# Kernel tuning notes

Hardware: AMD Instinct MI355X
Metric: run time of the kernel (lower is better)

Reference implementation:

```python
import jax, jax.numpy as jnp
import numpy as np

EMBED_DIM = 1024
NUM_HEADS = 16
HEAD_DIM = EMBED_DIM // NUM_HEADS


def setup_inputs() -> dict:
    key = jax.random.key(0)
    k_x, k_qw, k_qb, k_ow, k_ob = jax.random.split(key, 5)
    B, T, C = 2, 2048, EMBED_DIM
    scale = 1.0 / np.sqrt(C)
    return {
        "x": jax.random.normal(k_x, (B, T, C), dtype=jnp.float32),
        "qkv_w": jax.random.normal(k_qw, (C, 3 * C), dtype=jnp.float32) * scale,
        "qkv_b": jax.random.normal(k_qb, (3 * C,), dtype=jnp.float32) * 0.02,
        "out_w": jax.random.normal(k_ow, (C, C), dtype=jnp.float32) * scale,
        "out_b": jax.random.normal(k_ob, (C,), dtype=jnp.float32) * 0.02,
    }


def reference(x, qkv_w, qkv_b, out_w, out_b):
    # x: (B, T, C). Causal masked multi-head self-attention (eval mode: dropout off).
    B, T, C = x.shape
    H, Dh = NUM_HEADS, HEAD_DIM
    qkv = x @ qkv_w + qkv_b                      # (B, T, 3C)
    qkv = qkv.reshape(B, T, 3, H, Dh)
    q = jnp.transpose(qkv[:, :, 0], (0, 2, 1, 3))  # (B, H, T, Dh)
    k = jnp.transpose(qkv[:, :, 1], (0, 2, 1, 3))
    v = jnp.transpose(qkv[:, :, 2], (0, 2, 1, 3))
    scores = jnp.einsum("bhqd,bhkd->bhqk", q, k) / np.sqrt(Dh)
    causal = jnp.tril(jnp.ones((T, T), dtype=bool))
    scores = jnp.where(causal[None, None], scores, -jnp.inf)
    attn = jax.nn.softmax(scores, axis=-1)        # (B, H, T, T)
    out = jnp.einsum("bhqk,bhkd->bhqd", attn, v)  # (B, H, T, Dh)
    out = jnp.transpose(out, (0, 2, 1, 3)).reshape(B, T, C)
    return out @ out_w + out_b
```

## Files before the change

kernel.cpp:

```cpp
#include <hip/hip_runtime.h>


typedef __bf16 bf16;
typedef __attribute__((ext_vector_type(4))) __bf16 bf16x4;
typedef __attribute__((ext_vector_type(8))) __bf16 bf16x8;
typedef __attribute__((ext_vector_type(4))) float f32x4;

#define T_SEQ 2048
#define NHEAD 16
#define QSCALE 0.1803368801111244f

__device__ __forceinline__ void async16(const bf16* g, const bf16* l) {
    __builtin_amdgcn_global_load_lds(
        (const __attribute__((address_space(1))) void*)g,
        (__attribute__((address_space(3))) void*)l, 16, 0, 0);
}

__global__ __launch_bounds__(256) void prep(
    const float* __restrict__ x, bf16* __restrict__ xb,
    const float* __restrict__ qkv_w, bf16* __restrict__ wbT,
    const float* __restrict__ out_w, bf16* __restrict__ owbT) {
    const int bid = blockIdx.x, tid = threadIdx.x;
    if (bid < 4096) {
        int i = (bid * 256 + tid) * 4;
        float4 v = *(const float4*)(x + i);
        bf16x4 o;
        o.x = (bf16)v.x; o.y = (bf16)v.y; o.z = (bf16)v.z; o.w = (bf16)v.w;
        *(bf16x4*)(xb + i) = o;
        return;
    }
    __shared__ float tile[32][33];
    const float* in;
    bf16* out;
    int K_, N_, b;
    if (bid < 7168) { b = bid - 4096; in = qkv_w; out = wbT; K_ = 1024; N_ = 3072; }
    else            { b = bid - 7168; in = out_w; out = owbT; K_ = 1024; N_ = 1024; }
    int k0 = (b & 31) * 32, n0 = (b >> 5) * 32;
    int tx = tid & 31, ty = tid >> 5;
    for (int r = 0; r < 32; r += 8)
        tile[ty + r][tx] = in[(k0 + ty + r) * N_ + n0 + tx];
    __syncthreads();
    for (int r = 0; r < 32; r += 8)
        out[(n0 + ty + r) * K_ + k0 + tx] = (bf16)tile[tx][ty + r];
}


__global__ __launch_bounds__(256) void gemm_qkv(
    const bf16* __restrict__ A, const bf16* __restrict__ Bt,
    const float* __restrict__ bias,
    bf16* __restrict__ Qo, bf16* __restrict__ Ko, bf16* __restrict__ Vt) {
    __shared__ __align__(16) bf16 As[128 * 32];
    __shared__ __align__(16) bf16 Bs[128 * 32];
    const int t = threadIdx.x;
    const int lane = t & 63, wave = t >> 6;
    const int l15 = lane & 15, quad = lane >> 4;
    const int wm = wave & 1, wn = wave >> 1;
    const int m0 = blockIdx.y * 128, n0 = blockIdx.x * 128;

    f32x4 acc[4][4] = {};

    const bf16* ag = A + (m0 + (t >> 2)) * 1024 + (t & 3) * 8;
    const bf16* bg = Bt + (n0 + (t >> 2)) * 1024 + (t & 3) * 8;
    bf16* as0 = As + wave * 512;
    bf16* as1 = As + 2048 + wave * 512;
    bf16* bs0 = Bs + wave * 512;
    bf16* bs1 = Bs + 2048 + wave * 512;

    for (int k0 = 0; k0 < 1024; k0 += 32) {
        async16(ag + k0, as0);
        async16(ag + 64 * 1024 + k0, as1);
        async16(bg + k0, bs0);
        async16(bg + 64 * 1024 + k0, bs1);
        __syncthreads();
        bf16x8 af[4], bfr[4];
        for (int i = 0; i < 4; i++)
            af[i] = *(const bf16x8*)(As + (wm * 64 + i * 16 + l15) * 32 + quad * 8);
        for (int j = 0; j < 4; j++)
            bfr[j] = *(const bf16x8*)(Bs + (wn * 64 + j * 16 + l15) * 32 + quad * 8);
        for (int i = 0; i < 4; i++)
            for (int j = 0; j < 4; j++)
                acc[i][j] = __builtin_amdgcn_mfma_f32_16x16x32_bf16(af[i], bfr[j], acc[i][j], 0, 0, 0);
        __syncthreads();
    }

    for (int i = 0; i < 4; i++) {
        for (int j = 0; j < 4; j++) {
            int col = n0 + wn * 64 + j * 16 + l15;
            float bv = bias[col];
            int sec = col >> 10, c2 = col & 1023, h = c2 >> 6, d = c2 & 63;
            for (int r = 0; r < 4; r++) {
                int row = m0 + wm * 64 + i * 16 + quad * 4 + r;
                int b = row >> 11, tt = row & 2047;
                int bh = b * NHEAD + h;
                float v = acc[i][j][r] + bv;
                if (sec == 0)
                    Qo[(bh * T_SEQ + tt) * 64 + d] = (bf16)(v * QSCALE);
                else if (sec == 1)
                    Ko[(bh * T_SEQ + tt) * 64 + d] = (bf16)v;
                else
                    Vt[(bh * 64 + d) * T_SEQ + tt] = (bf16)v;
            }
        }
    }
}

#define PSTR 64
__global__ __launch_bounds__(512, 2) void attn(
    const bf16* __restrict__ Q, const bf16* __restrict__ K,
    const bf16* __restrict__ Vt, bf16* __restrict__ AO) {
    __shared__ __align__(16) bf16 Ks[2][64 * 64];
    __shared__ __align__(16) bf16 Vs[2][64 * 64];
    __shared__ __align__(16) bf16 Pb[8][16 * PSTR];
    const int tid = threadIdx.x;
    const int lane = tid & 63, wave = tid >> 6;
    const int l15 = lane & 15, quad = lane >> 4;
    const int bh = ((blockIdx.x & 7) << 2) | ((blockIdx.x >> 3) & 3);
    const int pr = blockIdx.x >> 5;

    const bf16* kp = K + bh * T_SEQ * 64;
    const bf16* vp = Vt + bh * 64 * T_SEQ;
    bf16* pw = &Pb[wave][0];
    const int b_ = bh >> 4, h_ = bh & 15;

    const int sx = (quad ^ (l15 & 7)) << 3;

    auto stage = [&](int kb, int b) {
        int rowi = tid >> 3, p = tid & 7;
        const bf16* ksrc = kp + (kb + rowi) * 64 + ((p ^ (rowi & 7)) << 3);
        async16(ksrc, &Ks[b][wave * 512]);
        const bf16* vsrc = vp + rowi * T_SEQ + kb + ((p ^ (rowi & 7)) << 3);
        async16(vsrc, &Vs[b][wave * 512]);
    };

    for (int half = 0; half < 2; half++) {
        const int qt = half ? pr : (15 - pr);
        const int t0 = qt * 128 + wave * 16;
        const int m = t0 >> 4;
        const bf16* qp = Q + (bh * T_SEQ + t0) * 64;
        bf16x8 qf0 = *(const bf16x8*)(qp + l15 * 64 + quad * 8);
        bf16x8 qf1 = *(const bf16x8*)(qp + l15 * 64 + 32 + quad * 8);

        f32x4 acc[4] = {};
        float lsum[4] = {0.f, 0.f, 0.f, 0.f};

        const int C = 2 * qt + 2;
        stage(0, 0);
        for (int c = 0; c < C; c++) {
            __syncthreads();
            if (c + 1 < C) stage((c + 1) * 64, (c + 1) & 1);
            const int nr = m - 4 * c + 1;
            if (nr > 0) {
                const int na = min(4, nr);
                const bool dg = (nr <= 4);
                const bf16* ksb = &Ks[c & 1][0];
                const bf16* vsb = &Vs[c & 1][0];

                f32x4 sc[4];
                for (int n = 0; n < 4; n++) {
                    if (n < na) {
                        const bf16* kbase = ksb + (n * 16 + l15) * 64;
                        bf16x8 kf0 = *(const bf16x8*)(kbase + sx);
                        bf16x8 kf1 = *(const bf16x8*)(kbase + (sx ^ 32));
                        f32x4 z = {};
                        z = __builtin_amdgcn_mfma_f32_16x16x32_bf16(qf0, kf0, z, 0, 0, 0);
                        z = __builtin_amdgcn_mfma_f32_16x16x32_bf16(qf1, kf1, z, 0, 0, 0);
                        sc[n] = z;
                    }
                }
                for (int n = 0; n < 4; n++) {
                    for (int r = 0; r < 4; r++) {
                        float e = 0.0f;
                        if (n < na) {
                            float v = sc[n][r];
                            if (dg && n == na - 1) {
                                int key = c * 64 + n * 16 + l15;
                                int qrow = t0 + quad * 4 + r;
                                if (key > qrow) v = -100000.0f;
                            }
                            e = __builtin_amdgcn_exp2f(v);
                        }
                        lsum[r] += e;
                        pw[(quad * 4 + r) * PSTR + n * 16 + l15] = (bf16)e;
                    }
                }
                __builtin_amdgcn_s_waitcnt(0xC07F);
                bf16x8 pf0 = *(const bf16x8*)(pw + l15 * PSTR + quad * 8);
                bf16x8 pf1 = *(const bf16x8*)(pw + l15 * PSTR + 32 + quad * 8);
                for (int j = 0; j < 4; j++) {
                    const bf16* vbase = vsb + (j * 16 + l15) * 64;
                    bf16x8 vf0 = *(const bf16x8*)(vbase + sx);
                    bf16x8 vf1 = *(const bf16x8*)(vbase + (sx ^ 32));
                    acc[j] = __builtin_amdgcn_mfma_f32_16x16x32_bf16(pf0, vf0, acc[j], 0, 0, 0);
                    acc[j] = __builtin_amdgcn_mfma_f32_16x16x32_bf16(pf1, vf1, acc[j], 0, 0, 0);
                }
            }
        }

        float linv[4];
        for (int r = 0; r < 4; r++) {
            float v = lsum[r];
            v += __shfl_xor(v, 1, 16);
            v += __shfl_xor(v, 2, 16);
            v += __shfl_xor(v, 4, 16);
            v += __shfl_xor(v, 8, 16);
            linv[r] = 1.0f / v;
        }
        bf16* aop = AO + (b_ * T_SEQ + t0) * 1024 + h_ * 64;
        for (int r = 0; r < 4; r++)
            for (int j = 0; j < 4; j++)
                aop[(quad * 4 + r) * 1024 + j * 16 + l15] = (bf16)(acc[j][r] * linv[r]);
    }
}

__global__ __launch_bounds__(256) void gemm_out_k(
    const bf16* __restrict__ A, const bf16* __restrict__ Bt,
    const float* __restrict__ bias, float* __restrict__ out) {
    __shared__ __align__(16) bf16 As[128 * 32];
    __shared__ __align__(16) bf16 Bs[128 * 32];
    const int t = threadIdx.x;
    const int lane = t & 63, wave = t >> 6;
    const int l15 = lane & 15, quad = lane >> 4;
    const int wm = wave & 1, wn = wave >> 1;
    const int m0 = blockIdx.y * 128, n0 = blockIdx.x * 128;

    f32x4 acc[4][4] = {};

    const bf16* ag = A + (m0 + (t >> 2)) * 1024 + (t & 3) * 8;
    const bf16* bg = Bt + (n0 + (t >> 2)) * 1024 + (t & 3) * 8;
    bf16* as0 = As + wave * 512;
    bf16* as1 = As + 2048 + wave * 512;
    bf16* bs0 = Bs + wave * 512;
    bf16* bs1 = Bs + 2048 + wave * 512;

    for (int k0 = 0; k0 < 1024; k0 += 32) {
        async16(ag + k0, as0);
        async16(ag + 64 * 1024 + k0, as1);
        async16(bg + k0, bs0);
        async16(bg + 64 * 1024 + k0, bs1);
        __syncthreads();
        bf16x8 af[4], bfr[4];
        for (int i = 0; i < 4; i++)
            af[i] = *(const bf16x8*)(As + (wm * 64 + i * 16 + l15) * 32 + quad * 8);
        for (int j = 0; j < 4; j++)
            bfr[j] = *(const bf16x8*)(Bs + (wn * 64 + j * 16 + l15) * 32 + quad * 8);
        for (int i = 0; i < 4; i++)
            for (int j = 0; j < 4; j++)
                acc[i][j] = __builtin_amdgcn_mfma_f32_16x16x32_bf16(af[i], bfr[j], acc[i][j], 0, 0, 0);
        __syncthreads();
    }

    for (int i = 0; i < 4; i++) {
        for (int j = 0; j < 4; j++) {
            int col = n0 + wn * 64 + j * 16 + l15;
            float bv = bias[col];
            for (int r = 0; r < 4; r++) {
                int row = m0 + wm * 64 + i * 16 + quad * 4 + r;
                out[row * 1024 + col] = acc[i][j][r] + bv;
            }
        }
    }
}

extern "C" void kernel_launch(void* const* d_in, const int* in_sizes, int n_in,
                              void* d_out, int out_size, void* d_ws, size_t ws_size,
                              hipStream_t stream) {
    const float* x     = (const float*)d_in[0];
    const float* qkv_w = (const float*)d_in[1];
    const float* qkv_b = (const float*)d_in[2];
    const float* out_w = (const float*)d_in[3];
    const float* out_b = (const float*)d_in[4];
    float* out = (float*)d_out;

    char* ws = (char*)d_ws;
    bf16* xb   = (bf16*)(ws);
    bf16* wbT  = (bf16*)(ws + (8ull << 20));
    bf16* owbT = (bf16*)(ws + (14ull << 20));
    bf16* Qb   = (bf16*)(ws + (16ull << 20));
    bf16* Kb   = (bf16*)(ws + (24ull << 20));
    bf16* Vt   = (bf16*)(ws + (32ull << 20));
    bf16* AO   = (bf16*)(ws + (40ull << 20));

    prep<<<8192, 256, 0, stream>>>(x, xb, qkv_w, wbT, out_w, owbT);
    gemm_qkv<<<dim3(24, 32), 256, 0, stream>>>(xb, wbT, qkv_b, Qb, Kb, Vt);
    attn<<<256, 512, 0, stream>>>(Qb, Kb, Vt, AO);
    gemm_out_k<<<dim3(8, 32), 256, 0, stream>>>(AO, owbT, out_b, out);
}
```

Measured before the change: 202.4 us.

## Split attention into 64-row query tiles with transposed score MFMA

The attention kernel now launches 1024 blocks of 256 threads, each owning one 64-row query tile, instead of 256 blocks of 512 threads that each processed two paired 128-row tiles. The score MFMA operands are swapped so each lane holds a key column, which lets the lane write probabilities as a packed bf16x4 into a padded LDS row and reduce row sums with two cross-quad shuffles. Diagonal blocks compute only the needed key subtiles per wave. This aims to raise occupancy and balance the causal workload at finer grain, at the cost of more K/V tile reloads per query row and more blocks to schedule.

```diff
diff --git a/kernel.cpp b/kernel.cpp
--- a/kernel.cpp
+++ b/kernel.cpp
@@ -43,7 +43,6 @@
     for (int r = 0; r < 32; r += 8)
         out[(n0 + ty + r) * K_ + k0 + tx] = (bf16)tile[tx][ty + r];
 }
-
 
 __global__ __launch_bounds__(256) void gemm_qkv(
     const bf16* __restrict__ A, const bf16* __restrict__ Bt,
@@ -104,111 +103,105 @@
     }
 }
 
-#define PSTR 64
-__global__ __launch_bounds__(512, 2) void attn(
+#define PST 80
+__global__ __launch_bounds__(256, 4) void attn(
     const bf16* __restrict__ Q, const bf16* __restrict__ K,
     const bf16* __restrict__ Vt, bf16* __restrict__ AO) {
     __shared__ __align__(16) bf16 Ks[2][64 * 64];
     __shared__ __align__(16) bf16 Vs[2][64 * 64];
-    __shared__ __align__(16) bf16 Pb[8][16 * PSTR];
+    __shared__ __align__(16) bf16 Pa[4][16 * PST];
     const int tid = threadIdx.x;
     const int lane = tid & 63, wave = tid >> 6;
     const int l15 = lane & 15, quad = lane >> 4;
-    const int bh = ((blockIdx.x & 7) << 2) | ((blockIdx.x >> 3) & 3);
-    const int pr = blockIdx.x >> 5;
+    const int xcdr = blockIdx.x & 7;
+    const int i_ = blockIdx.x >> 3;
+    const int bh = (xcdr << 2) | (i_ & 3);
+    const int ti = i_ >> 2;
+    const int qt = (ti & 1) ? (ti >> 1) : (31 - (ti >> 1));
+    const int t0w = qt * 64 + wave * 16;
 
     const bf16* kp = K + bh * T_SEQ * 64;
     const bf16* vp = Vt + bh * 64 * T_SEQ;
-    bf16* pw = &Pb[wave][0];
+    bf16* pw = &Pa[wave][0];
     const int b_ = bh >> 4, h_ = bh & 15;
 
     const int sx = (quad ^ (l15 & 7)) << 3;
 
+    const bf16* qp = Q + (bh * T_SEQ + t0w) * 64;
+    bf16x8 qf0 = *(const bf16x8*)(qp + l15 * 64 + quad * 8);
+    bf16x8 qf1 = *(const bf16x8*)(qp + l15 * 64 + 32 + quad * 8);
+
     auto stage = [&](int kb, int b) {
-        int rowi = tid >> 3, p = tid & 7;
-        const bf16* ksrc = kp + (kb + rowi) * 64 + ((p ^ (rowi & 7)) << 3);
-        async16(ksrc, &Ks[b][wave * 512]);
-        const bf16* vsrc = vp + rowi * T_SEQ + kb + ((p ^ (rowi & 7)) << 3);
-        async16(vsrc, &Vs[b][wave * 512]);
+        for (int i = 0; i < 2; i++) {
+            int row = i * 32 + (tid >> 3), p = tid & 7;
+            const bf16* ksrc = kp + (kb + row) * 64 + ((p ^ (row & 7)) << 3);
+            async16(ksrc, &Ks[b][i * 2048 + wave * 512]);
+            const bf16* vsrc = vp + row * T_SEQ + kb + ((p ^ (row & 7)) << 3);
+            async16(vsrc, &Vs[b][i * 2048 + wave * 512]);
+        }
     };
 
-    for (int half = 0; half < 2; half++) {
-        const int qt = half ? pr : (15 - pr);
-        const int t0 = qt * 128 + wave * 16;
-        const int m = t0 >> 4;
-        const bf16* qp = Q + (bh * T_SEQ + t0) * 64;
-        bf16x8 qf0 = *(const bf16x8*)(qp + l15 * 64 + quad * 8);
-        bf16x8 qf1 = *(const bf16x8*)(qp + l15 * 64 + 32 + quad * 8);
-
-        f32x4 acc[4] = {};
-        float lsum[4] = {0.f, 0.f, 0.f, 0.f};
-
-        const int C = 2 * qt + 2;
-        stage(0, 0);
-        for (int c = 0; c < C; c++) {
-            __syncthreads();
-            if (c + 1 < C) stage((c + 1) * 64, (c + 1) & 1);
-            const int nr = m - 4 * c + 1;
-            if (nr > 0) {
-                const int na = min(4, nr);
-                const bool dg = (nr <= 4);
-                const bf16* ksb = &Ks[c & 1][0];
-                const bf16* vsb = &Vs[c & 1][0];
-
-                f32x4 sc[4];
-                for (int n = 0; n < 4; n++) {
-                    if (n < na) {
-                        const bf16* kbase = ksb + (n * 16 + l15) * 64;
-                        bf16x8 kf0 = *(const bf16x8*)(kbase + sx);
-                        bf16x8 kf1 = *(const bf16x8*)(kbase + (sx ^ 32));
-                        f32x4 z = {};
-                        z = __builtin_amdgcn_mfma_f32_16x16x32_bf16(qf0, kf0, z, 0, 0, 0);
-                        z = __builtin_amdgcn_mfma_f32_16x16x32_bf16(qf1, kf1, z, 0, 0, 0);
-                        sc[n] = z;
-                    }
+    f32x4 acc[4] = {};
+    float lsum = 0.0f;
+
+    const int C = qt + 1;
+    stage(0, 0);
+    for (int c = 0; c < C; c++) {
+        __syncthreads();
+        if (c + 1 < C) stage((c + 1) * 64, (c + 1) & 1);
+        const bf16* ksb = &Ks[c & 1][0];
+        const bf16* vsb = &Vs[c & 1][0];
+        const bool dg = (c == qt);
+        const int na = dg ? (wave + 1) : 4;
+
+        f32x4 sc[4];
+        for (int n = 0; n < 4; n++) {
+            if (n < na) {
+                const bf16* kbase = ksb + (n * 16 + l15) * 64;
+                bf16x8 kf0 = *(const bf16x8*)(kbase + sx);
+                bf16x8 kf1 = *(const bf16x8*)(kbase + (sx ^ 32));
+                f32x4 z = {};
+                z = __builtin_amdgcn_mfma_f32_16x16x32_bf16(kf0, qf0, z, 0, 0, 0);
+                z = __builtin_amdgcn_mfma_f32_16x16x32_bf16(kf1, qf1, z, 0, 0, 0);
+                sc[n] = z;
+            }
+        }
+        for (int n = 0; n < 4; n++) {
+            bf16x4 pv;
+            if (n < na) {
+                const bool dmask = dg && (n == na - 1);
+                for (int r = 0; r < 4; r++) {
+                    float v = sc[n][r];
+                    if (dmask && (quad * 4 + r > l15)) v = -100000.0f;
+                    float e = __builtin_amdgcn_exp2f(v);
+                    lsum += e;
+                    pv[r] = (bf16)e;
                 }
-                for (int n = 0; n < 4; n++) {
-                    for (int r = 0; r < 4; r++) {
-                        float e = 0.0f;
-                        if (n < na) {
-                            float v = sc[n][r];
-                            if (dg && n == na - 1) {
-                                int key = c * 64 + n * 16 + l15;
-                                int qrow = t0 + quad * 4 + r;
-                                if (key > qrow) v = -100000.0f;
-                            }
-                            e = __builtin_amdgcn_exp2f(v);
-                        }
-                        lsum[r] += e;
-                        pw[(quad * 4 + r) * PSTR + n * 16 + l15] = (bf16)e;
-                    }
-                }
-                __builtin_amdgcn_s_waitcnt(0xC07F);
-                bf16x8 pf0 = *(const bf16x8*)(pw + l15 * PSTR + quad * 8);
-                bf16x8 pf1 = *(const bf16x8*)(pw + l15 * PSTR + 32 + quad * 8);
-                for (int j = 0; j < 4; j++) {
-                    const bf16* vbase = vsb + (j * 16 + l15) * 64;
-                    bf16x8 vf0 = *(const bf16x8*)(vbase + sx);
-                    bf16x8 vf1 = *(const bf16x8*)(vbase + (sx ^ 32));
-                    acc[j] = __builtin_amdgcn_mfma_f32_16x16x32_bf16(pf0, vf0, acc[j], 0, 0, 0);
-                    acc[j] = __builtin_amdgcn_mfma_f32_16x16x32_bf16(pf1, vf1, acc[j], 0, 0, 0);
-                }
-            }
-        }
-
-        float linv[4];
-        for (int r = 0; r < 4; r++) {
-            float v = lsum[r];
-            v += __shfl_xor(v, 1, 16);
-            v += __shfl_xor(v, 2, 16);
-            v += __shfl_xor(v, 4, 16);
-            v += __shfl_xor(v, 8, 16);
-            linv[r] = 1.0f / v;
-        }
-        bf16* aop = AO + (b_ * T_SEQ + t0) * 1024 + h_ * 64;
-        for (int r = 0; r < 4; r++)
-            for (int j = 0; j < 4; j++)
-                aop[(quad * 4 + r) * 1024 + j * 16 + l15] = (bf16)(acc[j][r] * linv[r]);
+            } else {
+                pv[0] = pv[1] = pv[2] = pv[3] = (bf16)0.0f;
+            }
+            *(bf16x4*)(pw + l15 * PST + n * 16 + quad * 4) = pv;
+        }
+        __builtin_amdgcn_s_waitcnt(0xC07F);
+        for (int g = 0; g < 2; g++) {
+            bf16x8 pf = *(const bf16x8*)(pw + l15 * PST + g * 32 + quad * 8);
+            for (int j = 0; j < 4; j++) {
+                const bf16* vbase = vsb + (j * 16 + l15) * 64;
+                bf16x8 vf = *(const bf16x8*)(vbase + (g ? (sx ^ 32) : sx));
+                acc[j] = __builtin_amdgcn_mfma_f32_16x16x32_bf16(pf, vf, acc[j], 0, 0, 0);
+            }
+        }
+    }
+
+    lsum += __shfl_xor(lsum, 16);
+    lsum += __shfl_xor(lsum, 32);
+    float linv = 1.0f / lsum;
+
+    bf16* aop = AO + (b_ * T_SEQ + t0w) * 1024 + h_ * 64;
+    for (int r = 0; r < 4; r++) {
+        float lr = __shfl(linv, quad * 4 + r, 16);
+        for (int j = 0; j < 4; j++)
+            aop[(quad * 4 + r) * 1024 + j * 16 + l15] = (bf16)(acc[j][r] * lr);
     }
 }
 
@@ -282,6 +275,6 @@
 
     prep<<<8192, 256, 0, stream>>>(x, xb, qkv_w, wbT, out_w, owbT);
     gemm_qkv<<<dim3(24, 32), 256, 0, stream>>>(xb, wbT, qkv_b, Qb, Kb, Vt);
-    attn<<<256, 512, 0, stream>>>(Qb, Kb, Vt, AO);
+    attn<<<1024, 256, 0, stream>>>(Qb, Kb, Vt, AO);
     gemm_out_k<<<dim3(8, 32), 256, 0, stream>>>(AO, owbT, out_b, out);
 }
```

After: 188.2 us. 1.08x faster.
